# Kernel tuning notes

Measured on AMD Instinct MI355X. Metric: run time of the kernel, lower is better.

The kernel has to match this reference:

```python
import jax, jax.numpy as jnp
import numpy as np

N = 50000
E = 800000
F_IN = 256
HEADS = 4
C = 64
NEG_SLOPE = 0.2


def setup_inputs() -> dict:
    key = jax.random.key(0)
    ks = jax.random.split(key, 7)
    x = jax.random.normal(ks[0], (N, F_IN), dtype=jnp.float32)
    edge_index = jax.random.randint(ks[1], (2, E), 0, N, dtype=jnp.int64)
    # Glorot-ish scaling for weights
    W = jax.random.normal(ks[2], (F_IN, HEADS * C), dtype=jnp.float32) / np.sqrt(F_IN)
    att_src = jax.random.normal(ks[3], (HEADS, C), dtype=jnp.float32) / np.sqrt(C)
    att_dst = jax.random.normal(ks[4], (HEADS, C), dtype=jnp.float32) / np.sqrt(C)
    bias = jnp.zeros((HEADS * C,), dtype=jnp.float32)
    prelu_a = jnp.full((1,), 0.25, dtype=jnp.float32)  # PReLU default init
    return {"x": x, "edge_index": edge_index, "W": W, "att_src": att_src,
            "att_dst": att_dst, "bias": bias, "prelu_a": prelu_a}


def _gat_forward(x, edge_index, W, att_src, att_dst, bias, prelu_a):
    n = x.shape[0]
    # add self loops (PyG GATConv default)
    loops = jnp.arange(n, dtype=edge_index.dtype)
    src = jnp.concatenate([edge_index[0], loops])  # message source j
    dst = jnp.concatenate([edge_index[1], loops])  # message target i

    h = (x @ W).reshape(n, HEADS, C)                    # [N,H,C]
    a_src = jnp.einsum('nhc,hc->nh', h, att_src)        # [N,H]
    a_dst = jnp.einsum('nhc,hc->nh', h, att_dst)        # [N,H]

    e = a_src[src] + a_dst[dst]                         # [Etot,H]
    e = jnp.where(e >= 0, e, NEG_SLOPE * e)             # LeakyReLU(0.2)

    # numerically stable softmax over edges grouped by destination node
    m = jax.ops.segment_max(e, dst, num_segments=n)     # [N,H]
    alpha = jnp.exp(e - m[dst])
    denom = jax.ops.segment_sum(alpha, dst, num_segments=n)
    alpha = alpha / (denom[dst] + 1e-16)                # [Etot,H]

    msg = alpha[:, :, None] * h[src]                    # [Etot,H,C]
    out = jax.ops.segment_sum(msg, dst, num_segments=n) # [N,H,C]
    out = out.reshape(n, HEADS * C) + bias
    # PReLU with single shared parameter
    return jnp.where(out >= 0, out, prelu_a * out)


def reference(x, edge_index, W, att_src, att_dst, bias, prelu_a):
    return _gat_forward(x, edge_index, W, att_src, att_dst, bias, prelu_a)
```

## Files before the change

kernel.cpp:

```cpp
#include <hip/hip_runtime.h>
#include <stdint.h>


using u16 = unsigned short;
typedef float f32x4 __attribute__((ext_vector_type(4)));
typedef __bf16 bf16x8 __attribute__((ext_vector_type(8)));
typedef u16 u16x8 __attribute__((ext_vector_type(8)));

#define NEG 0.2f
#define APAD 264
#define NBLK1 256

__device__ __forceinline__ float bf2f(u16 u) {
    union { uint32_t i; float f; } v; v.i = ((uint32_t)u) << 16; return v.f;
}
__device__ __forceinline__ u16 f2bf(float f) {
    union { float f; uint32_t i; } v; v.f = f;
    uint32_t r = v.i + 0x7FFFu + ((v.i >> 16) & 1u);
    return (u16)(r >> 16);
}
__device__ __forceinline__ void split2(float f, u16& h, u16& l) {
    union { float f; uint32_t i; } v; v.f = f;
    h = (u16)(v.i >> 16);
    float r = f - bf2f(h);
    union { float f; uint32_t i; } w; w.f = r;
    l = (u16)(w.i >> 16);
}
__device__ __forceinline__ float wexp(float e) {
    e = e >= 0.f ? e : NEG * e;
    return __expf(e);
}

__global__ __launch_bounds__(256) void prep_kernel(
    const float* __restrict__ W, u16* __restrict__ Wfh, u16* __restrict__ Wfl,
    const int* __restrict__ edst, int* __restrict__ cnt1,
    int E, int Nn, int chunk)
{
    __shared__ int h1[256];
    const int tid = threadIdx.x, cb = blockIdx.x;
    h1[tid] = 0;
    __syncthreads();
    const int e0 = cb * chunk;
    const int e1 = (e0 + chunk < E) ? e0 + chunk : E;
    for (int e = e0 + tid; e < e1; e += 256) {
        int i = edst[e];
        i = ((unsigned)i < (unsigned)Nn) ? i : 0;
        atomicAdd(&h1[i >> 8], 1);
    }
    __syncthreads();
    cnt1[cb * 256 + tid] = h1[tid];

    if (cb < 32) {
        const int f = cb * 4 + (tid >> 6);
        const int l = tid & 63;
        const int kg = f >> 4, nb = f & 15;
        const int n = nb * 16 + (l & 15);
        const int kb = kg * 32 + (l >> 4) * 8;
        u16x8 hv, lv;
#pragma unroll
        for (int j = 0; j < 8; j++) {
            u16 th, tl;
            split2(W[(size_t)(kb + j) * 256 + n], th, tl);
            hv[j] = th;
            lv[j] = tl;
        }
        *(u16x8*)(Wfh + ((size_t)f * 64 + l) * 8) = hv;
        *(u16x8*)(Wfl + ((size_t)f * 64 + l) * 8) = lv;
    }
}

__global__ __launch_bounds__(256, 2) void mix_kernel(
    const float* __restrict__ X, const u16* __restrict__ Wfh,
    const u16* __restrict__ Wfl, const float* __restrict__ attS,
    const float* __restrict__ attD, u16* __restrict__ H,
    float* __restrict__ a_src, float* __restrict__ a_dst,
    const int* __restrict__ esrc, const int* __restrict__ edst,
    const int* __restrict__ cnt1, uint32_t* __restrict__ part,
    int E, int Nn, int chunk)
{
    __shared__ u16 Ah[64 * APAD];
    __shared__ u16 Al[64 * APAD];
    __shared__ int cur[256];
    __shared__ int wsum[4];
    const int tid = threadIdx.x;
    const int ln = tid & 63, wv = tid >> 6;

    if (blockIdx.x < NBLK1) {
        const int cb = blockIdx.x;
        int pre = 0, tot = 0;
        for (int c = 0; c < NBLK1; c++) {
            const int v = cnt1[c * 256 + tid];
            tot += v;
            pre += (c < cb) ? v : 0;
        }
        int s = tot;
#pragma unroll
        for (int o = 1; o < 64; o <<= 1) {
            int u = __shfl_up(s, o, 64);
            if (ln >= o) s += u;
        }
        if (ln == 63) wsum[wv] = s;
        __syncthreads();
        int wpre = 0;
#pragma unroll
        for (int w2 = 0; w2 < 4; w2++) wpre += (w2 < wv) ? wsum[w2] : 0;
        cur[tid] = (wpre + s - tot) + pre;
        __syncthreads();
        const int e0 = cb * chunk;
        const int e1 = (e0 + chunk < E) ? e0 + chunk : E;
        for (int e = e0 + tid; e < e1; e += 256) {
            int i = edst[e];
            i = ((unsigned)i < (unsigned)Nn) ? i : 0;
            int j = esrc[e];
            j = ((unsigned)j < (unsigned)Nn) ? j : 0;
            const int pos = atomicAdd(&cur[i >> 8], 1);
            part[pos] = (uint32_t)j | ((uint32_t)(i & 255) << 16);
        }
        return;
    }

    const int m0 = (blockIdx.x - NBLK1) * 64;
    const int wave = tid >> 6, lane = tid & 63;
    const int quad = lane >> 4, lr = lane & 15;

#pragma unroll
    for (int i = 0; i < 16; i++) {
        const int f = i * 256 + tid;
        const int row = f >> 6;
        const int c4 = (f & 63) * 4;
        int grow = m0 + row;
        if (grow >= Nn) grow = Nn - 1;
        const float4 v = *(const float4*)(X + (size_t)grow * 256 + c4);
        u16 h0, l0, h1, l1, h2, l2, h3, l3;
        split2(v.x, h0, l0); split2(v.y, h1, l1);
        split2(v.z, h2, l2); split2(v.w, h3, l3);
        uint2 hp, lp;
        hp.x = (uint32_t)h0 | ((uint32_t)h1 << 16);
        hp.y = (uint32_t)h2 | ((uint32_t)h3 << 16);
        lp.x = (uint32_t)l0 | ((uint32_t)l1 << 16);
        lp.y = (uint32_t)l2 | ((uint32_t)l3 << 16);
        *(uint2*)(Ah + row * APAD + c4) = hp;
        *(uint2*)(Al + row * APAD + c4) = lp;
    }
    __syncthreads();

    f32x4 acc[4][4] = {};
    bf16x8 bh[2][4], bl[2][4];

#pragma unroll
    for (int ni = 0; ni < 4; ni++) {
        const size_t o = ((size_t)(wave * 4 + ni) * 64 + lane) * 8;
        bh[0][ni] = *(const bf16x8*)(Wfh + o);
        bl[0][ni] = *(const bf16x8*)(Wfl + o);
    }

#pragma unroll
    for (int kg = 0; kg < 8; kg++) {
        const int st = kg & 1, ns = st ^ 1;
        if (kg < 7) {
#pragma unroll
            for (int ni = 0; ni < 4; ni++) {
                const size_t o = ((size_t)((kg + 1) * 16 + wave * 4 + ni) * 64 + lane) * 8;
                bh[ns][ni] = *(const bf16x8*)(Wfh + o);
                bl[ns][ni] = *(const bf16x8*)(Wfl + o);
            }
        }
        bf16x8 ah[4], al[4];
#pragma unroll
        for (int mi = 0; mi < 4; mi++) {
            const int o = (mi * 16 + lr) * APAD + kg * 32 + quad * 8;
            ah[mi] = *(const bf16x8*)(Ah + o);
            al[mi] = *(const bf16x8*)(Al + o);
        }
#pragma unroll
        for (int ni = 0; ni < 4; ni++)
#pragma unroll
            for (int mi = 0; mi < 4; mi++) {
                acc[mi][ni] = __builtin_amdgcn_mfma_f32_16x16x32_bf16(
                    ah[mi], bh[st][ni], acc[mi][ni], 0, 0, 0);
                acc[mi][ni] = __builtin_amdgcn_mfma_f32_16x16x32_bf16(
                    ah[mi], bl[st][ni], acc[mi][ni], 0, 0, 0);
                acc[mi][ni] = __builtin_amdgcn_mfma_f32_16x16x32_bf16(
                    al[mi], bh[st][ni], acc[mi][ni], 0, 0, 0);
            }
    }

    {
        float asv[4], adv[4];
#pragma unroll
        for (int ni = 0; ni < 4; ni++) {
            asv[ni] = attS[wave * 64 + ni * 16 + lr];
            adv[ni] = attD[wave * 64 + ni * 16 + lr];
        }
#pragma unroll
        for (int mi = 0; mi < 4; mi++)
#pragma unroll
            for (int r = 0; r < 4; r++) {
                float ps = 0.f, pd = 0.f;
#pragma unroll
                for (int ni = 0; ni < 4; ni++) {
                    ps += acc[mi][ni][r] * asv[ni];
                    pd += acc[mi][ni][r] * adv[ni];
                }
#pragma unroll
                for (int off = 8; off >= 1; off >>= 1) {
                    ps += __shfl_xor(ps, off, 16);
                    pd += __shfl_xor(pd, off, 16);
                }
                if (lr == 0) {
                    const int row = m0 + mi * 16 + quad * 4 + r;
                    if (row < Nn) {
                        a_src[row * 4 + wave] = ps;
                        a_dst[row * 4 + wave] = pd;
                    }
                }
            }
    }

    __syncthreads();
    const int n0 = wave * 64;
#pragma unroll
    for (int mi = 0; mi < 4; mi++)
#pragma unroll
        for (int ni = 0; ni < 4; ni++) {
            const int col = n0 + ni * 16 + lr;
#pragma unroll
            for (int r = 0; r < 4; r++)
                Ah[(mi * 16 + quad * 4 + r) * APAD + col] = f2bf(acc[mi][ni][r]);
        }
    __syncthreads();
#pragma unroll
    for (int swp = 0; swp < 8; swp++) {
        const int idx = swp * 256 + tid;
        const int row = idx >> 5;
        const int c16 = idx & 31;
        const int grow = m0 + row;
        if (grow < Nn)
            *(u16x8*)(H + (size_t)grow * 256 + c16 * 8) =
                *(const u16x8*)(Ah + row * APAD + c16 * 8);
    }
}

__global__ __launch_bounds__(256) void p2_kernel(
    const uint32_t* __restrict__ part, const int* __restrict__ cnt1,
    int* __restrict__ deg, int* __restrict__ offs, int* __restrict__ csr_src,
    int E, int Nn, int nb1)
{
    __shared__ int lds[256];
    __shared__ int wsum[4];
    __shared__ int sbd[2];
    const int b = blockIdx.x, tid = threadIdx.x;
    const int ln = tid & 63, wv = tid >> 6;

    int tot = 0;
    for (int c = 0; c < NBLK1; c++) tot += cnt1[c * 256 + tid];
    int s = tot;
#pragma unroll
    for (int o = 1; o < 64; o <<= 1) {
        int u = __shfl_up(s, o, 64);
        if (ln >= o) s += u;
    }
    if (ln == 63) wsum[wv] = s;
    __syncthreads();
    int wpre = 0;
#pragma unroll
    for (int w2 = 0; w2 < 4; w2++) wpre += (w2 < wv) ? wsum[w2] : 0;
    if (tid == b) { sbd[0] = wpre + s - tot; sbd[1] = wpre + s; }
    __syncthreads();
    const int bstart = sbd[0], bend = sbd[1];

    lds[tid] = 0;
    __syncthreads();
    for (int e = bstart + tid; e < bend; e += 256)
        atomicAdd(&lds[part[e] >> 16], 1);
    __syncthreads();
    const int cnt = lds[tid];
    int s2 = cnt;
#pragma unroll
    for (int o = 1; o < 64; o <<= 1) {
        int u = __shfl_up(s2, o, 64);
        if (ln >= o) s2 += u;
    }
    if (ln == 63) wsum[wv] = s2;
    __syncthreads();
    int wpre2 = 0;
#pragma unroll
    for (int w2 = 0; w2 < 4; w2++) wpre2 += (w2 < wv) ? wsum[w2] : 0;
    const int ex = bstart + wpre2 + s2 - cnt;
    const int node = (b << 8) + tid;
    if (node < Nn) { deg[node] = cnt; offs[node] = ex; }
    __syncthreads();
    lds[tid] = ex;
    __syncthreads();
    for (int e = bstart + tid; e < bend; e += 256) {
        const uint32_t pr = part[e];
        const int pos = atomicAdd(&lds[pr >> 16], 1);
        csr_src[pos] = (int)(pr & 0xFFFFu);
    }
}

__global__ __launch_bounds__(256) void gather_kernel(
    const u16* __restrict__ H, const int* __restrict__ offs,
    const int* __restrict__ deg, const int* __restrict__ csr_src,
    const float* __restrict__ a_src, const float* __restrict__ a_dst,
    const float* __restrict__ bias, const float* __restrict__ prelu,
    float* __restrict__ out, int Nn)
{
    const int wave = threadIdx.x >> 6, lane = threadIdx.x & 63;
    const int g = blockIdx.x >> 3, s = blockIdx.x & 7;
    const int head = s >> 1;
    const int node = ((g << 1) + (s & 1)) * 4 + wave;
    if (node >= Nn) return;
    const int p = lane >> 5;
    const int cp2 = lane & 31;
    const int ch = (head << 6) + cp2 * 2;

    const float adv = a_dst[node * 4 + head];
    const float ws = wexp(a_src[node * 4 + head] + adv);
    const uint32_t hself = *(const uint32_t*)(H + (size_t)node * 256 + ch);
    float acc0 = 0.f, acc1 = 0.f, sumw = 0.f;

    const int d = deg[node];
    const int* __restrict__ cp = csr_src + offs[node];

    for (int k = 0; k < d; k += 64) {
        const int q = d - k;
        const int es = (lane < q) ? lane : q - 1;
        const int jj = cp[k + es];
        float ww = wexp(a_src[jj * 4 + head] + adv);
        ww = (lane < q) ? ww : 0.f;
        sumw += ww;
#pragma unroll
        for (int g0 = 0; g0 < 64; g0 += 16) {
            if (g0 >= q) break;
            uint32_t hv[8];
#pragma unroll
            for (int i = 0; i < 8; i++) {
                const int r = g0 + 2 * i + p;
                const int jt = __shfl(jj, r, 64);
                hv[i] = *(const uint32_t*)(H + ((size_t)jt << 8) + ch);
            }
#pragma unroll
            for (int i = 0; i < 8; i++) {
                const int r = g0 + 2 * i + p;
                const float w = __shfl(ww, r, 64);
                acc0 += w * bf2f((u16)hv[i]);
                acc1 += w * bf2f((u16)(hv[i] >> 16));
            }
        }
    }
    acc0 += __shfl_xor(acc0, 32, 64);
    acc1 += __shfl_xor(acc1, 32, 64);
#pragma unroll
    for (int off = 32; off >= 1; off >>= 1)
        sumw += __shfl_xor(sumw, off, 64);

    if (p == 0) {
        const float inv = 1.f / (ws + sumw + 1e-16f);
        const float pa = prelu[0];
        float o0 = (acc0 + ws * bf2f((u16)hself)) * inv + bias[ch];
        float o1 = (acc1 + ws * bf2f((u16)(hself >> 16))) * inv + bias[ch + 1];
        o0 = o0 >= 0.f ? o0 : pa * o0;
        o1 = o1 >= 0.f ? o1 : pa * o1;
        float2 ov; ov.x = o0; ov.y = o1;
        *(float2*)(out + (size_t)node * 256 + ch) = ov;
    }
}

extern "C" void kernel_launch(void* const* d_in, const int* in_sizes, int n_in,
                              void* d_out, int out_size, void* d_ws, size_t ws_size,
                              hipStream_t stream)
{
    const float* X    = (const float*)d_in[0];
    const int*   EI   = (const int*)d_in[1];
    const float* W    = (const float*)d_in[2];
    const float* attS = (const float*)d_in[3];
    const float* attD = (const float*)d_in[4];
    const float* bias = (const float*)d_in[5];
    const float* pa   = (const float*)d_in[6];

    const int Nn = in_sizes[0] / 256;
    const int E  = in_sizes[1] / 2;
    const int* esrc = EI;
    const int* edst = EI + E;

    const int nb1   = (Nn + 255) >> 8;
    const int chunk = (E + NBLK1 - 1) / NBLK1;

    char* p = (char*)d_ws;
    u16*      H       = (u16*)p;      p += (size_t)Nn * 256 * 2;
    float*    a_src   = (float*)p;    p += (size_t)Nn * 4 * 4;
    float*    a_dst   = (float*)p;    p += (size_t)Nn * 4 * 4;
    u16*      Wfh     = (u16*)p;      p += 256 * 256 * 2;
    u16*      Wfl     = (u16*)p;      p += 256 * 256 * 2;
    int*      deg     = (int*)p;      p += (size_t)Nn * 4;
    int*      offs    = (int*)p;      p += (size_t)Nn * 4;
    int*      cnt1    = (int*)p;      p += (size_t)NBLK1 * 256 * 4;
    uint32_t* part    = (uint32_t*)p; p += (size_t)E * 4;
    int*      csr_src = (int*)p;      p += ((size_t)E + 16) * 4;

    prep_kernel<<<NBLK1, 256, 0, stream>>>(W, Wfh, Wfl, edst, cnt1,
                                           E, Nn, chunk);
    const int gemmBlocks = (Nn + 63) / 64;
    mix_kernel<<<NBLK1 + gemmBlocks, 256, 0, stream>>>(
        X, Wfh, Wfl, attS, attD, H, a_src, a_dst,
        esrc, edst, cnt1, part, E, Nn, chunk);
    p2_kernel<<<nb1, 256, 0, stream>>>(part, cnt1, deg, offs, csr_src,
                                       E, Nn, nb1);
    const int gblocks = ((Nn + 7) / 8) * 8;
    gather_kernel<<<gblocks, 256, 0, stream>>>(H, offs, deg, csr_src,
                                               a_src, a_dst, bias, pa,
                                               (float*)d_out, Nn);
}
```

Baseline: 255.2 us.

## Shrink GEMM tile to 32 rows and rewrite gather as one wave per node

The GEMM block now covers 32 rows instead of 64, which halves LDS use and drops the two-blocks-per-CU launch bound so more blocks can be resident. The gather kernel is restructured: each wave handles a whole node across all four heads, with each lane owning 4 channels. Each lane walks the neighbour list serially with 8-wide unrolled loads, replacing the per-head block split and cross-lane shuffles. This makes H row reads wider and more coalesced and removes the shuffle reductions. In exchange, every lane redundantly loads the index and recomputes the exp weight, and the per-node loop is serial over degree.

New measurement: 227.9 us. -10.7%, faster.

```diff
diff --git a/kernel.cpp b/kernel.cpp
--- a/kernel.cpp
+++ b/kernel.cpp
@@ -69,7 +69,7 @@
     }
 }
 
-__global__ __launch_bounds__(256, 2) void mix_kernel(
+__global__ __launch_bounds__(256) void mix_kernel(
     const float* __restrict__ X, const u16* __restrict__ Wfh,
     const u16* __restrict__ Wfl, const float* __restrict__ attS,
     const float* __restrict__ attD, u16* __restrict__ H,
@@ -78,8 +78,8 @@
     const int* __restrict__ cnt1, uint32_t* __restrict__ part,
     int E, int Nn, int chunk)
 {
-    __shared__ u16 Ah[64 * APAD];
-    __shared__ u16 Al[64 * APAD];
+    __shared__ u16 Ah[32 * APAD];
+    __shared__ u16 Al[32 * APAD];
     __shared__ int cur[256];
     __shared__ int wsum[4];
     const int tid = threadIdx.x;
@@ -119,12 +119,12 @@
         return;
     }
 
-    const int m0 = (blockIdx.x - NBLK1) * 64;
+    const int m0 = (blockIdx.x - NBLK1) * 32;
     const int wave = tid >> 6, lane = tid & 63;
     const int quad = lane >> 4, lr = lane & 15;
 
 #pragma unroll
-    for (int i = 0; i < 16; i++) {
+    for (int i = 0; i < 8; i++) {
         const int f = i * 256 + tid;
         const int row = f >> 6;
         const int c4 = (f & 63) * 4;
@@ -144,7 +144,7 @@
     }
     __syncthreads();
 
-    f32x4 acc[4][4] = {};
+    f32x4 acc[2][4] = {};
     bf16x8 bh[2][4], bl[2][4];
 
 #pragma unroll
@@ -165,9 +165,9 @@
                 bl[ns][ni] = *(const bf16x8*)(Wfl + o);
             }
         }
-        bf16x8 ah[4], al[4];
-#pragma unroll
-        for (int mi = 0; mi < 4; mi++) {
+        bf16x8 ah[2], al[2];
+#pragma unroll
+        for (int mi = 0; mi < 2; mi++) {
             const int o = (mi * 16 + lr) * APAD + kg * 32 + quad * 8;
             ah[mi] = *(const bf16x8*)(Ah + o);
             al[mi] = *(const bf16x8*)(Al + o);
@@ -175,7 +175,7 @@
 #pragma unroll
         for (int ni = 0; ni < 4; ni++)
 #pragma unroll
-            for (int mi = 0; mi < 4; mi++) {
+            for (int mi = 0; mi < 2; mi++) {
                 acc[mi][ni] = __builtin_amdgcn_mfma_f32_16x16x32_bf16(
                     ah[mi], bh[st][ni], acc[mi][ni], 0, 0, 0);
                 acc[mi][ni] = __builtin_amdgcn_mfma_f32_16x16x32_bf16(
@@ -193,7 +193,7 @@
             adv[ni] = attD[wave * 64 + ni * 16 + lr];
         }
 #pragma unroll
-        for (int mi = 0; mi < 4; mi++)
+        for (int mi = 0; mi < 2; mi++)
 #pragma unroll
             for (int r = 0; r < 4; r++) {
                 float ps = 0.f, pd = 0.f;
@@ -220,7 +220,7 @@
     __syncthreads();
     const int n0 = wave * 64;
 #pragma unroll
-    for (int mi = 0; mi < 4; mi++)
+    for (int mi = 0; mi < 2; mi++)
 #pragma unroll
         for (int ni = 0; ni < 4; ni++) {
             const int col = n0 + ni * 16 + lr;
@@ -230,7 +230,7 @@
         }
     __syncthreads();
 #pragma unroll
-    for (int swp = 0; swp < 8; swp++) {
+    for (int swp = 0; swp < 4; swp++) {
         const int idx = swp * 256 + tid;
         const int row = idx >> 5;
         const int c16 = idx & 31;
@@ -307,64 +307,78 @@
     float* __restrict__ out, int Nn)
 {
     const int wave = threadIdx.x >> 6, lane = threadIdx.x & 63;
-    const int g = blockIdx.x >> 3, s = blockIdx.x & 7;
-    const int head = s >> 1;
-    const int node = ((g << 1) + (s & 1)) * 4 + wave;
+    const int node = blockIdx.x * 4 + wave;
     if (node >= Nn) return;
-    const int p = lane >> 5;
-    const int cp2 = lane & 31;
-    const int ch = (head << 6) + cp2 * 2;
+    const int head = lane >> 4;
+    const int c = lane * 4;
 
     const float adv = a_dst[node * 4 + head];
-    const float ws = wexp(a_src[node * 4 + head] + adv);
-    const uint32_t hself = *(const uint32_t*)(H + (size_t)node * 256 + ch);
-    float acc0 = 0.f, acc1 = 0.f, sumw = 0.f;
-
+    float acc0, acc1, acc2, acc3, sumw;
+    {
+        float ws = wexp(a_src[node * 4 + head] + adv);
+        uint2 hv = *(const uint2*)(H + (size_t)node * 256 + c);
+        acc0 = ws * bf2f((u16)hv.x);
+        acc1 = ws * bf2f((u16)(hv.x >> 16));
+        acc2 = ws * bf2f((u16)hv.y);
+        acc3 = ws * bf2f((u16)(hv.y >> 16));
+        sumw = ws;
+    }
+    const int start = offs[node];
     const int d = deg[node];
-    const int* __restrict__ cp = csr_src + offs[node];
-
-    for (int k = 0; k < d; k += 64) {
-        const int q = d - k;
-        const int es = (lane < q) ? lane : q - 1;
-        const int jj = cp[k + es];
-        float ww = wexp(a_src[jj * 4 + head] + adv);
-        ww = (lane < q) ? ww : 0.f;
-        sumw += ww;
-#pragma unroll
-        for (int g0 = 0; g0 < 64; g0 += 16) {
-            if (g0 >= q) break;
-            uint32_t hv[8];
-#pragma unroll
-            for (int i = 0; i < 8; i++) {
-                const int r = g0 + 2 * i + p;
-                const int jt = __shfl(jj, r, 64);
-                hv[i] = *(const uint32_t*)(H + ((size_t)jt << 8) + ch);
-            }
-#pragma unroll
-            for (int i = 0; i < 8; i++) {
-                const int r = g0 + 2 * i + p;
-                const float w = __shfl(ww, r, 64);
-                acc0 += w * bf2f((u16)hv[i]);
-                acc1 += w * bf2f((u16)(hv[i] >> 16));
-            }
-        }
-    }
-    acc0 += __shfl_xor(acc0, 32, 64);
-    acc1 += __shfl_xor(acc1, 32, 64);
-#pragma unroll
-    for (int off = 32; off >= 1; off >>= 1)
-        sumw += __shfl_xor(sumw, off, 64);
-
-    if (p == 0) {
-        const float inv = 1.f / (ws + sumw + 1e-16f);
-        const float pa = prelu[0];
-        float o0 = (acc0 + ws * bf2f((u16)hself)) * inv + bias[ch];
-        float o1 = (acc1 + ws * bf2f((u16)(hself >> 16))) * inv + bias[ch + 1];
-        o0 = o0 >= 0.f ? o0 : pa * o0;
-        o1 = o1 >= 0.f ? o1 : pa * o1;
-        float2 ov; ov.x = o0; ov.y = o1;
-        *(float2*)(out + (size_t)node * 256 + ch) = ov;
-    }
+    int k = 0;
+    for (; k + 8 <= d; k += 8) {
+        int j[8]; uint2 hv[8]; float w[8];
+#pragma unroll
+        for (int q = 0; q < 8; q++) j[q] = csr_src[start + k + q];
+#pragma unroll
+        for (int q = 0; q < 8; q++) hv[q] = *(const uint2*)(H + (size_t)j[q] * 256 + c);
+#pragma unroll
+        for (int q = 0; q < 8; q++) w[q] = wexp(a_src[j[q] * 4 + head] + adv);
+#pragma unroll
+        for (int q = 0; q < 8; q++) {
+            acc0 += w[q] * bf2f((u16)hv[q].x);
+            acc1 += w[q] * bf2f((u16)(hv[q].x >> 16));
+            acc2 += w[q] * bf2f((u16)hv[q].y);
+            acc3 += w[q] * bf2f((u16)(hv[q].y >> 16));
+            sumw += w[q];
+        }
+    }
+    for (; k + 4 <= d; k += 4) {
+        int j[4]; uint2 hv[4]; float w[4];
+#pragma unroll
+        for (int q = 0; q < 4; q++) j[q] = csr_src[start + k + q];
+#pragma unroll
+        for (int q = 0; q < 4; q++) hv[q] = *(const uint2*)(H + (size_t)j[q] * 256 + c);
+#pragma unroll
+        for (int q = 0; q < 4; q++) w[q] = wexp(a_src[j[q] * 4 + head] + adv);
+#pragma unroll
+        for (int q = 0; q < 4; q++) {
+            acc0 += w[q] * bf2f((u16)hv[q].x);
+            acc1 += w[q] * bf2f((u16)(hv[q].x >> 16));
+            acc2 += w[q] * bf2f((u16)hv[q].y);
+            acc3 += w[q] * bf2f((u16)(hv[q].y >> 16));
+            sumw += w[q];
+        }
+    }
+    for (; k < d; k++) {
+        const int j = csr_src[start + k];
+        const uint2 hv = *(const uint2*)(H + (size_t)j * 256 + c);
+        const float w = wexp(a_src[j * 4 + head] + adv);
+        acc0 += w * bf2f((u16)hv.x);
+        acc1 += w * bf2f((u16)(hv.x >> 16));
+        acc2 += w * bf2f((u16)hv.y);
+        acc3 += w * bf2f((u16)(hv.y >> 16));
+        sumw += w;
+    }
+    const float inv = 1.f / (sumw + 1e-16f);
+    const float pa = prelu[0];
+    const float4 bv = *(const float4*)(bias + c);
+    float4 ov;
+    ov.x = acc0 * inv + bv.x; ov.x = ov.x >= 0.f ? ov.x : pa * ov.x;
+    ov.y = acc1 * inv + bv.y; ov.y = ov.y >= 0.f ? ov.y : pa * ov.y;
+    ov.z = acc2 * inv + bv.z; ov.z = ov.z >= 0.f ? ov.z : pa * ov.z;
+    ov.w = acc3 * inv + bv.w; ov.w = ov.w >= 0.f ? ov.w : pa * ov.w;
+    *(float4*)(out + (size_t)node * 256 + c) = ov;
 }
 
 extern "C" void kernel_launch(void* const* d_in, const int* in_sizes, int n_in,
@@ -401,14 +415,13 @@
 
     prep_kernel<<<NBLK1, 256, 0, stream>>>(W, Wfh, Wfl, edst, cnt1,
                                            E, Nn, chunk);
-    const int gemmBlocks = (Nn + 63) / 64;
+    const int gemmBlocks = (Nn + 31) / 32;
     mix_kernel<<<NBLK1 + gemmBlocks, 256, 0, stream>>>(
         X, Wfh, Wfl, attS, attD, H, a_src, a_dst,
         esrc, edst, cnt1, part, E, Nn, chunk);
     p2_kernel<<<nb1, 256, 0, stream>>>(part, cnt1, deg, offs, csr_src,
                                        E, Nn, nb1);
-    const int gblocks = ((Nn + 7) / 8) * 8;
-    gather_kernel<<<gblocks, 256, 0, stream>>>(H, offs, deg, csr_src,
-                                               a_src, a_dst, bias, pa,
-                                               (float*)d_out, Nn);
-}
+    gather_kernel<<<(Nn + 3) / 4, 256, 0, stream>>>(H, offs, deg, csr_src,
+                                                    a_src, a_dst, bias, pa,
+                                                    (float*)d_out, Nn);
+}
```
